# Performance work log

Hardware: AMD Instinct MI355X
Metric: run time of the kernel (lower is better)

The kernel has to match this reference:

```python
import jax, jax.numpy as jnp
import numpy as np
from jax import lax

# shifts generated by _generate_shifts(kernel_size=3): (s1, s2) pairs with
# (s1, s2) >= (0, 0) lexicographically, excluding (0, 0)
SHIFTS = [(0, 1), (1, -1), (1, 0), (1, 1)]


def conv2d_same(x, w, b):
    # x: (B, C_in, H, W), w: (C_out, C_in, kH, kW), b: (C_out,)
    y = lax.conv_general_dilated(
        x, w, window_strides=(1, 1), padding='SAME',
        dimension_numbers=('NCHW', 'OIHW', 'NCHW'))
    return y + b[None, :, None, None]


def setup_inputs() -> dict:
    key = jax.random.key(0)
    k1, k2, k3, k4, k5 = jax.random.split(key, 5)
    B, C_in, C_out, H, W, K = 8, 64, 64, 256, 256, 3
    fan = C_in * K * K
    return {
        'x': jax.random.normal(k1, (B, C_in, H, W), dtype=jnp.float32),
        'w1': jax.random.normal(k2, (C_out, C_in, K, K), dtype=jnp.float32) / np.sqrt(fan),
        'b1': jax.random.normal(k3, (C_out,), dtype=jnp.float32) * 0.01,
        'w2': jax.random.normal(k4, (C_out, C_in, K, K), dtype=jnp.float32) / np.sqrt(fan),
        'b2': jax.random.normal(k5, (C_out,), dtype=jnp.float32) * 0.01,
    }


def reference(x, w1, b1, w2, b2):
    linear_term = conv2d_same(x, w1, b1)
    # torch.roll(x, shifts=(shift_y, shift_x), dims=(2,3)) with
    # circular_shift(x, s1, s2) -> shift_x=s1, shift_y=s2.
    # conv2 is linear, so sum_i conv2(prod_i) == conv2(sum_i prod_i)
    # with the bias added once per shift.
    quad_in = jnp.zeros_like(x)
    for s1, s2 in SHIFTS:
        x_shifted = jnp.roll(x, shift=(s2, s1), axis=(2, 3))
        quad_in = quad_in + jnp.clip(x * x_shifted, -1.0, 1.0)
    quadratic_term = conv2d_same(quad_in, w2, b2 * float(len(SHIFTS)))
    return linear_term + quadratic_term
```

## Files before the change

kernel.cpp:

```cpp
#include <hip/hip_runtime.h>
#include <stdint.h>


typedef short s16x8 __attribute__((ext_vector_type(8)));
typedef float f32x4 __attribute__((ext_vector_type(4)));

__device__ __forceinline__ float clip1(float v) { return fminf(fmaxf(v, -1.f), 1.f); }

__device__ __forceinline__ unsigned short f2bf(float f) {
    union { float f; unsigned u; } v; v.f = f;
    unsigned u = v.u;
    return (unsigned short)((u + 0x7fffu + ((u >> 16) & 1u)) >> 16);
}

__device__ __forceinline__ float bf2f(unsigned short u) {
    union { unsigned v; float f; } t; t.v = ((unsigned)u) << 16; return t.f;
}

__device__ __forceinline__ void gload16(const void* g, void* l) {
    __builtin_amdgcn_global_load_lds(
        (const __attribute__((address_space(1))) unsigned int*)g,
        (__attribute__((address_space(3))) unsigned int*)l, 16, 0, 0);
}

__global__ void prep_w(const float* __restrict__ w1, const float* __restrict__ w2,
                       unsigned short* __restrict__ Wb) {
    int idx = blockIdx.x * 256 + threadIdx.x;
    int kk = idx % 96;
    int rest = idx / 96;
    int co = rest & 63; rest >>= 6;
    int cc = rest & 3;
    int kh = rest >> 2;
    int kw = kk >> 5;
    int cci = kk & 31;
    int c2 = cc * 32 + cci;
    const float* src = (c2 < 64) ? w1 : w2;
    int ci = c2 & 63;
    Wb[idx] = f2bf(src[((co * 64 + ci) * 3 + kh) * 3 + kw]);
}

__global__ __launch_bounds__(512, 1) void prep_u2(const float* __restrict__ x,
                                                  unsigned short* __restrict__ U) {
    __shared__ unsigned short X[3][64][268];
    int bid = blockIdx.x;
    int bh = ((bid & 7) << 8) + (bid >> 3);
    int b = bh >> 8, h = bh & 255;
    int tid = threadIdx.x;

    for (int it = 0; it < 24; ++it) {
        int idx = tid + (it << 9);
        int w4 = idx & 63;
        int c  = (idx >> 6) & 63;
        int r  = idx >> 12;
        int gr = (h + r + 255) & 255;
        const float4 v = *(const float4*)(x + (((size_t)(b * 64 + c)) << 16)
                                            + (gr << 8) + (w4 << 2));
        ushort4 p;
        p.x = f2bf(v.x); p.y = f2bf(v.y); p.z = f2bf(v.z); p.w = f2bf(v.w);
        *(ushort4*)&X[r][c][w4 << 2] = p;
    }
    __syncthreads();

    int c  = tid & 63;
    int wv = tid >> 6;
    int p0 = wv << 5;
    int pm0 = (p0 + 255) & 255;
    float pxc = bf2f(X[1][c][pm0]);
    float pxu = bf2f(X[0][c][pm0]);
    float pxd = bf2f(X[2][c][pm0]);
    size_t base = ((size_t)bh) << 8;
#pragma unroll 4
    for (int i = 0; i < 32; ++i) {
        int p = p0 + i;
        unsigned short xcb = X[1][c][p];
        float xc = bf2f(xcb);
        float xu = bf2f(X[0][c][p]);
        float xd = bf2f(X[2][c][p]);
        float q = clip1(xc * xu) + clip1(xc * pxd) + clip1(xc * pxc) + clip1(xc * pxu);
        size_t po = (base + p) << 7;
        U[po + c]      = xcb;
        U[po + 64 + c] = f2bf(q);
        pxc = xc; pxu = xu; pxd = xd;
    }
}

__global__ __launch_bounds__(512, 2) void conv6(
        const unsigned short* __restrict__ U,
        const unsigned short* __restrict__ Wb,
        const float* __restrict__ b1, const float* __restrict__ b2,
        float* __restrict__ out) {
    __shared__ unsigned short Alds[3][64][96];
    __shared__ unsigned short Ib[2][6][130][32];

    int bid = blockIdx.x;
    int logical = ((bid & 7) << 7) + (bid >> 3);
    int b = logical >> 7;
    int rem = logical & 127;
    int h0 = (rem >> 1) << 2;
    int whalf = rem & 1;
    int w0 = whalf << 7;
    int tid = threadIdx.x;
    int wid = tid >> 6;
    int ln = tid & 63;
    int lr = ln & 15;
    int lq = ln >> 4;
    int rowsel = wid >> 1;
    int pq = wid & 1;
    int o = h0 + rowsel;

    const size_t ubase = ((size_t)b) << 23;

    f32x4 acc[4][4];
#pragma unroll
    for (int m = 0; m < 4; m++)
#pragma unroll
        for (int n = 0; n < 4; n++) {
            acc[m][n][0] = 0.f; acc[m][n][1] = 0.f; acc[m][n][2] = 0.f; acc[m][n][3] = 0.f;
        }

    auto stage_input = [&](int ccx, int nb) {
        const unsigned short* ub = U + ubase + ccx * 32;
#pragma unroll
        for (int ir = 0; ir < 6; ++ir) {
            int r = h0 - 1 + ir;
            if (r < 0 || r > 255) continue;
            int p = 1 + (tid >> 2), q = tid & 3;
            const unsigned short* g = ub + (((size_t)r) << 15)
                                        + (((size_t)(w0 + p - 1)) << 7) + q * 8;
            unsigned short* l = &Ib[nb][ir][1][0] + (size_t)wid * 512;
            gload16(g, l);
        }
    };
    auto stage_weights = [&](int ccx) {
#pragma unroll
        for (int k = 0; k < 5; ++k) {
            int J = k * 512 + tid;
            if (J < 2304) {
                int kh = J / 768;
                int remw = J - kh * 768;
                const unsigned short* g = Wb + (size_t)(kh * 4 + ccx) * 6144 + remw * 8;
                unsigned short* l = ((unsigned short*)Alds) + (size_t)(k * 512 + wid * 64) * 8;
                gload16(g, l);
            }
        }
    };
    auto fix_edges = [&](int ccx, int nb) {
        if (tid < 48) {
            int ir = tid >> 3, rest = tid & 7;
            int side = rest >> 2, q = rest & 3;
            int p = side ? 129 : 0;
            int gcol = side ? (w0 + 128) : (w0 - 1);
            int r = h0 - 1 + ir;
            uint4 v = make_uint4(0u, 0u, 0u, 0u);
            if (gcol >= 0 && gcol <= 255 && r >= 0 && r <= 255)
                v = *(const uint4*)(U + ubase + (((size_t)r) << 15)
                                    + (((size_t)gcol) << 7) + ccx * 32 + q * 8);
            *(uint4*)&Ib[nb][ir][p][q * 8] = v;
        }
        if (h0 == 0)
            for (int i = tid; i < 520; i += 512)
                *(uint4*)&Ib[nb][0][i >> 2][(i & 3) * 8] = make_uint4(0u, 0u, 0u, 0u);
        if (h0 == 252)
            for (int i = tid; i < 520; i += 512)
                *(uint4*)&Ib[nb][5][i >> 2][(i & 3) * 8] = make_uint4(0u, 0u, 0u, 0u);
    };

    stage_input(0, 0);
    stage_weights(0);
    fix_edges(0, 0);
    __syncthreads();

    int cur = 0;
    for (int cc = 0; cc < 4; ++cc) {
        if (cc < 3) stage_input(cc + 1, cur ^ 1);
        __builtin_amdgcn_s_setprio(1);
#pragma unroll
        for (int kh = 0; kh < 3; ++kh) {
            int ir = rowsel + kh;
#pragma unroll
            for (int kw = 0; kw < 3; ++kw) {
                s16x8 af[4], bfr[4];
#pragma unroll
                for (int m = 0; m < 4; m++)
                    af[m] = *(const s16x8*)&Alds[kh][m * 16 + lr][kw * 32 + lq * 8];
#pragma unroll
                for (int n = 0; n < 4; n++)
                    bfr[n] = *(const s16x8*)&Ib[cur][ir][(pq << 6) + n * 16 + lr + kw][lq * 8];
#pragma unroll
                for (int m = 0; m < 4; m++)
#pragma unroll
                    for (int n = 0; n < 4; n++)
                        acc[m][n] = __builtin_amdgcn_mfma_f32_16x16x32_bf16(af[m], bfr[n], acc[m][n], 0, 0, 0);
            }
        }
        __builtin_amdgcn_s_setprio(0);
        __syncthreads();
        if (cc < 3) {
            stage_weights(cc + 1);
            fix_edges(cc + 1, cur ^ 1);
            __syncthreads();
            cur ^= 1;
        }
    }

#pragma unroll
    for (int m = 0; m < 4; m++) {
#pragma unroll
        for (int jj = 0; jj < 4; jj++) {
            int co = m * 16 + lq * 4 + jj;
            float bias = b1[co] + 4.f * b2[co];
#pragma unroll
            for (int n = 0; n < 4; n++) {
                int wpix = w0 + (pq << 6) + n * 16 + lr;
                out[(((size_t)(b * 64 + co)) << 16) + (o << 8) + wpix] = acc[m][n][jj] + bias;
            }
        }
    }
}

__global__ void fallback_conv(const float* __restrict__ x,
                              const float* __restrict__ w1, const float* __restrict__ b1,
                              const float* __restrict__ w2, const float* __restrict__ b2,
                              float* __restrict__ out) {
    size_t idx = (size_t)blockIdx.x * 256 + threadIdx.x;
    int w = idx & 255;
    int h = (int)(idx >> 8) & 255;
    int co = (int)(idx >> 16) & 63;
    int b = (int)(idx >> 22);
    float acc = b1[co] + 4.f * b2[co];
    const float* xb = x + (((size_t)b * 64) << 16);
    for (int ci = 0; ci < 64; ci++) {
        const float* xp = xb + (((size_t)ci) << 16);
        for (int kh = 0; kh < 3; kh++) {
            int hh = h + kh - 1;
            if (hh < 0 || hh > 255) continue;
            for (int kw = 0; kw < 3; kw++) {
                int ww = w + kw - 1;
                if (ww < 0 || ww > 255) continue;
                float xv = xp[(hh << 8) + ww];
                float g1 = w1[((co * 64 + ci) * 3 + kh) * 3 + kw];
                float g2 = w2[((co * 64 + ci) * 3 + kh) * 3 + kw];
                int hm = (hh + 255) & 255, hp = (hh + 1) & 255, wm = (ww + 255) & 255;
                float q = clip1(xv * xp[(hm << 8) + ww]) + clip1(xv * xp[(hp << 8) + wm])
                        + clip1(xv * xp[(hh << 8) + wm]) + clip1(xv * xp[(hm << 8) + wm]);
                acc = fmaf(g1, xv, acc);
                acc = fmaf(g2, q, acc);
            }
        }
    }
    out[idx] = acc;
}

extern "C" void kernel_launch(void* const* d_in, const int* in_sizes, int n_in,
                              void* d_out, int out_size, void* d_ws, size_t ws_size,
                              hipStream_t stream) {
    const float* x  = (const float*)d_in[0];
    const float* w1 = (const float*)d_in[1];
    const float* b1 = (const float*)d_in[2];
    const float* w2 = (const float*)d_in[3];
    const float* b2 = (const float*)d_in[4];
    float* out = (float*)d_out;

    const size_t WB_BYTES = 262144;
    const size_t U_BYTES  = (size_t)8 * 256 * 256 * 128 * 2;
    if (ws_size >= WB_BYTES + U_BYTES) {
        unsigned short* Wb = (unsigned short*)d_ws;
        unsigned short* U  = (unsigned short*)((char*)d_ws + WB_BYTES);
        prep_w<<<dim3(288), dim3(256), 0, stream>>>(w1, w2, Wb);
        prep_u2<<<dim3(2048), dim3(512), 0, stream>>>(x, U);
        conv6<<<dim3(1024), dim3(512), 0, stream>>>(U, Wb, b1, b2, out);
    } else {
        fallback_conv<<<dim3(131072), dim3(256), 0, stream>>>(x, w1, b1, w2, b2, out);
    }
}
```

Before: 174.3 us.

## XOR-swizzle LDS layouts for weight and input tiles in conv kernel

```diff
diff --git a/kernel.cpp b/kernel.cpp
--- a/kernel.cpp
+++ b/kernel.cpp
@@ -24,19 +24,23 @@
 }
 
 __global__ void prep_w(const float* __restrict__ w1, const float* __restrict__ w2,
-                       unsigned short* __restrict__ Wb) {
+                       unsigned short* __restrict__ Wb2) {
     int idx = blockIdx.x * 256 + threadIdx.x;
-    int kk = idx % 96;
-    int rest = idx / 96;
-    int co = rest & 63; rest >>= 6;
-    int cc = rest & 3;
-    int kh = rest >> 2;
-    int kw = kk >> 5;
-    int cci = kk & 31;
-    int c2 = cc * 32 + cci;
-    const float* src = (c2 < 64) ? w1 : w2;
-    int ci = c2 & 63;
-    Wb[idx] = f2bf(src[((co * 64 + ci) * 3 + kh) * 3 + kw]);
+    int sh   = idx & 7;
+    int beta = (idx >> 3) & 15;
+    int co   = (idx >> 7) & 63;
+    int cc   = (idx >> 13) & 3;
+    int kh   = idx >> 15;
+    int blk  = beta ^ (co & 7);
+    float val = 0.f;
+    if (blk < 12) {
+        int kw = blk >> 2;
+        int lq = blk & 3;
+        int c2 = cc * 32 + lq * 8 + sh;
+        const float* src = (c2 < 64) ? w1 : w2;
+        val = src[((co * 64 + (c2 & 63)) * 3 + kh) * 3 + kw];
+    }
+    Wb2[idx] = f2bf(val);
 }
 
 __global__ __launch_bounds__(512, 1) void prep_u2(const float* __restrict__ x,
@@ -84,13 +88,13 @@
     }
 }
 
-__global__ __launch_bounds__(512, 2) void conv6(
+__global__ __launch_bounds__(512, 2) void conv7(
         const unsigned short* __restrict__ U,
-        const unsigned short* __restrict__ Wb,
+        const unsigned short* __restrict__ Wb2,
         const float* __restrict__ b1, const float* __restrict__ b2,
         float* __restrict__ out) {
-    __shared__ unsigned short Alds[3][64][96];
-    __shared__ unsigned short Ib[2][6][130][32];
+    __shared__ unsigned short Alds[3][64][128];
+    __shared__ unsigned short Ib[2][6][4160];
 
     int bid = blockIdx.x;
     int logical = ((bid & 7) << 7) + (bid >> 3);
@@ -107,8 +111,15 @@
     int rowsel = wid >> 1;
     int pq = wid & 1;
     int o = h0 + rowsel;
-
     const size_t ubase = ((size_t)b) << 23;
+
+    int D   = 64 + wid * 1024 + ln * 16;
+    int su  = D >> 7;
+    int stv = ((D >> 4) & 7) ^ (su & 7);
+    int sp  = 2 * su + (stv >> 2);
+    int slq = stv & 3;
+    int scol = w0 - 1 + sp;
+    const unsigned short* usrc0 = U + ubase + (((size_t)scol) << 7) + slq * 8;
 
     f32x4 acc[4][4];
 #pragma unroll
@@ -119,50 +130,45 @@
         }
 
     auto stage_input = [&](int ccx, int nb) {
-        const unsigned short* ub = U + ubase + ccx * 32;
 #pragma unroll
         for (int ir = 0; ir < 6; ++ir) {
             int r = h0 - 1 + ir;
             if (r < 0 || r > 255) continue;
-            int p = 1 + (tid >> 2), q = tid & 3;
-            const unsigned short* g = ub + (((size_t)r) << 15)
-                                        + (((size_t)(w0 + p - 1)) << 7) + q * 8;
-            unsigned short* l = &Ib[nb][ir][1][0] + (size_t)wid * 512;
+            const unsigned short* g = usrc0 + (((size_t)r) << 15) + ccx * 32;
+            void* l = (char*)&Ib[nb][ir][0] + 64 + wid * 1024;
             gload16(g, l);
         }
     };
     auto stage_weights = [&](int ccx) {
 #pragma unroll
-        for (int k = 0; k < 5; ++k) {
-            int J = k * 512 + tid;
-            if (J < 2304) {
-                int kh = J / 768;
-                int remw = J - kh * 768;
-                const unsigned short* g = Wb + (size_t)(kh * 4 + ccx) * 6144 + remw * 8;
-                unsigned short* l = ((unsigned short*)Alds) + (size_t)(k * 512 + wid * 64) * 8;
-                gload16(g, l);
-            }
+        for (int k = 0; k < 6; ++k) {
+            int j = k * 512 + tid;
+            int kh = j >> 10;
+            int remw = j & 1023;
+            const unsigned short* g = Wb2 + (((size_t)(kh * 4 + ccx)) << 13) + remw * 8;
+            void* l = (char*)Alds + (size_t)(k * 512 + wid * 64) * 16;
+            gload16(g, l);
         }
     };
     auto fix_edges = [&](int ccx, int nb) {
         if (tid < 48) {
-            int ir = tid >> 3, rest = tid & 7;
-            int side = rest >> 2, q = rest & 3;
-            int p = side ? 129 : 0;
+            int ir = tid >> 3, r2 = tid & 7;
+            int side = r2 >> 2, q = r2 & 3;
             int gcol = side ? (w0 + 128) : (w0 - 1);
             int r = h0 - 1 + ir;
             uint4 v = make_uint4(0u, 0u, 0u, 0u);
             if (gcol >= 0 && gcol <= 255 && r >= 0 && r <= 255)
                 v = *(const uint4*)(U + ubase + (((size_t)r) << 15)
                                     + (((size_t)gcol) << 7) + ccx * 32 + q * 8);
-            *(uint4*)&Ib[nb][ir][p][q * 8] = v;
+            int off = side ? (8192 + (4 + q) * 16) : (q * 16);
+            *(uint4*)((char*)&Ib[nb][ir][0] + off) = v;
         }
         if (h0 == 0)
             for (int i = tid; i < 520; i += 512)
-                *(uint4*)&Ib[nb][0][i >> 2][(i & 3) * 8] = make_uint4(0u, 0u, 0u, 0u);
+                *(uint4*)((char*)&Ib[nb][0][0] + i * 16) = make_uint4(0u, 0u, 0u, 0u);
         if (h0 == 252)
             for (int i = tid; i < 520; i += 512)
-                *(uint4*)&Ib[nb][5][i >> 2][(i & 3) * 8] = make_uint4(0u, 0u, 0u, 0u);
+                *(uint4*)((char*)&Ib[nb][5][0] + i * 16) = make_uint4(0u, 0u, 0u, 0u);
     };
 
     stage_input(0, 0);
@@ -172,20 +178,29 @@
 
     int cur = 0;
     for (int cc = 0; cc < 4; ++cc) {
-        if (cc < 3) stage_input(cc + 1, cur ^ 1);
+        if (cc < 3) {
+            stage_input(cc + 1, cur ^ 1);
+            fix_edges(cc + 1, cur ^ 1);
+        }
         __builtin_amdgcn_s_setprio(1);
 #pragma unroll
         for (int kh = 0; kh < 3; ++kh) {
             int ir = rowsel + kh;
+            const char* ibb = (const char*)&Ib[cur][ir][0];
 #pragma unroll
             for (int kw = 0; kw < 3; ++kw) {
                 s16x8 af[4], bfr[4];
+                int slot = ((kw << 2) | lq) ^ (lr & 7);
 #pragma unroll
                 for (int m = 0; m < 4; m++)
-                    af[m] = *(const s16x8*)&Alds[kh][m * 16 + lr][kw * 32 + lq * 8];
-#pragma unroll
-                for (int n = 0; n < 4; n++)
-                    bfr[n] = *(const s16x8*)&Ib[cur][ir][(pq << 6) + n * 16 + lr + kw][lq * 8];
+                    af[m] = *(const s16x8*)&Alds[kh][m * 16 + lr][slot * 8];
+#pragma unroll
+                for (int n = 0; n < 4; n++) {
+                    int p = (pq << 6) + n * 16 + lr + kw;
+                    int u = p >> 1;
+                    int s = (((p & 1) << 2) | lq) ^ (u & 7);
+                    bfr[n] = *(const s16x8*)(ibb + u * 128 + s * 16);
+                }
 #pragma unroll
                 for (int m = 0; m < 4; m++)
 #pragma unroll
@@ -197,7 +212,6 @@
         __syncthreads();
         if (cc < 3) {
             stage_weights(cc + 1);
-            fix_edges(cc + 1, cur ^ 1);
             __syncthreads();
             cur ^= 1;
         }
@@ -264,11 +278,11 @@
     const size_t WB_BYTES = 262144;
     const size_t U_BYTES  = (size_t)8 * 256 * 256 * 128 * 2;
     if (ws_size >= WB_BYTES + U_BYTES) {
-        unsigned short* Wb = (unsigned short*)d_ws;
-        unsigned short* U  = (unsigned short*)((char*)d_ws + WB_BYTES);
-        prep_w<<<dim3(288), dim3(256), 0, stream>>>(w1, w2, Wb);
+        unsigned short* Wb2 = (unsigned short*)d_ws;
+        unsigned short* U   = (unsigned short*)((char*)d_ws + WB_BYTES);
+        prep_w<<<dim3(384), dim3(256), 0, stream>>>(w1, w2, Wb2);
         prep_u2<<<dim3(2048), dim3(512), 0, stream>>>(x, U);
-        conv6<<<dim3(1024), dim3(512), 0, stream>>>(U, Wb, b1, b2, out);
+        conv7<<<dim3(1024), dim3(512), 0, stream>>>(U, Wb2, b1, b2, out);
     } else {
         fallback_conv<<<dim3(131072), dim3(256), 0, stream>>>(x, w1, b1, w2, b2, out);
     }
```

Measured after the change: 172.8 us. No clear change (-0.9%).

## Shrink conv tile, read weights from global, swizzle LDS input layout

Applied to the files above, without the earlier changes.

```diff
diff --git a/kernel.cpp b/kernel.cpp
--- a/kernel.cpp
+++ b/kernel.cpp
@@ -84,31 +84,32 @@
     }
 }
 
-__global__ __launch_bounds__(512, 2) void conv6(
+__global__ __launch_bounds__(256, 3) void conv8(
         const unsigned short* __restrict__ U,
         const unsigned short* __restrict__ Wb,
         const float* __restrict__ b1, const float* __restrict__ b2,
         float* __restrict__ out) {
-    __shared__ unsigned short Alds[3][64][96];
-    __shared__ unsigned short Ib[2][6][130][32];
+    __shared__ unsigned short Ib[6][2112];
 
     int bid = blockIdx.x;
-    int logical = ((bid & 7) << 7) + (bid >> 3);
-    int b = logical >> 7;
-    int rem = logical & 127;
-    int h0 = (rem >> 1) << 2;
-    int whalf = rem & 1;
-    int w0 = whalf << 7;
+    int logical = ((bid & 7) << 8) + (bid >> 3);
+    int b = logical >> 8;
+    int rem = logical & 255;
+    int h0 = (rem >> 2) << 2;
+    int w0 = (rem & 3) << 6;
     int tid = threadIdx.x;
     int wid = tid >> 6;
     int ln = tid & 63;
     int lr = ln & 15;
     int lq = ln >> 4;
-    int rowsel = wid >> 1;
-    int pq = wid & 1;
-    int o = h0 + rowsel;
-
+    int o = h0 + wid;
     const size_t ubase = ((size_t)b) << 23;
+
+    int D16 = 4 + (wid << 6) + ln;
+    int su  = D16 >> 3;
+    int stv = (D16 & 7) ^ (su & 7);
+    int pp  = 2 * su + (stv >> 2);
+    const size_t colbase = (((size_t)(w0 - 1 + pp)) << 7) + (size_t)((stv & 3) * 8);
 
     f32x4 acc[4][4];
 #pragma unroll
@@ -118,88 +119,71 @@
             acc[m][n][0] = 0.f; acc[m][n][1] = 0.f; acc[m][n][2] = 0.f; acc[m][n][3] = 0.f;
         }
 
-    auto stage_input = [&](int ccx, int nb) {
-        const unsigned short* ub = U + ubase + ccx * 32;
+    auto stage = [&](int ccx) {
 #pragma unroll
         for (int ir = 0; ir < 6; ++ir) {
             int r = h0 - 1 + ir;
             if (r < 0 || r > 255) continue;
-            int p = 1 + (tid >> 2), q = tid & 3;
-            const unsigned short* g = ub + (((size_t)r) << 15)
-                                        + (((size_t)(w0 + p - 1)) << 7) + q * 8;
-            unsigned short* l = &Ib[nb][ir][1][0] + (size_t)wid * 512;
-            gload16(g, l);
-        }
-    };
-    auto stage_weights = [&](int ccx) {
-#pragma unroll
-        for (int k = 0; k < 5; ++k) {
-            int J = k * 512 + tid;
-            if (J < 2304) {
-                int kh = J / 768;
-                int remw = J - kh * 768;
-                const unsigned short* g = Wb + (size_t)(kh * 4 + ccx) * 6144 + remw * 8;
-                unsigned short* l = ((unsigned short*)Alds) + (size_t)(k * 512 + wid * 64) * 8;
-                gload16(g, l);
-            }
-        }
-    };
-    auto fix_edges = [&](int ccx, int nb) {
+            const unsigned short* g = U + ubase + (((size_t)r) << 15) + colbase + ccx * 32;
+            gload16(g, (char*)&Ib[ir][0] + 64 + (wid << 10));
+        }
         if (tid < 48) {
-            int ir = tid >> 3, rest = tid & 7;
-            int side = rest >> 2, q = rest & 3;
-            int p = side ? 129 : 0;
-            int gcol = side ? (w0 + 128) : (w0 - 1);
+            int ir = tid >> 3, r2 = tid & 7;
+            int side = r2 >> 2, q = r2 & 3;
+            int gcol = side ? (w0 + 64) : (w0 - 1);
             int r = h0 - 1 + ir;
             uint4 v = make_uint4(0u, 0u, 0u, 0u);
             if (gcol >= 0 && gcol <= 255 && r >= 0 && r <= 255)
                 v = *(const uint4*)(U + ubase + (((size_t)r) << 15)
                                     + (((size_t)gcol) << 7) + ccx * 32 + q * 8);
-            *(uint4*)&Ib[nb][ir][p][q * 8] = v;
+            *(uint4*)((char*)&Ib[ir][0] + (side ? 4160 : 0) + q * 16) = v;
         }
         if (h0 == 0)
-            for (int i = tid; i < 520; i += 512)
-                *(uint4*)&Ib[nb][0][i >> 2][(i & 3) * 8] = make_uint4(0u, 0u, 0u, 0u);
+            for (int i = tid; i < 264; i += 256)
+                *(uint4*)((char*)&Ib[0][0] + i * 16) = make_uint4(0u, 0u, 0u, 0u);
         if (h0 == 252)
-            for (int i = tid; i < 520; i += 512)
-                *(uint4*)&Ib[nb][5][i >> 2][(i & 3) * 8] = make_uint4(0u, 0u, 0u, 0u);
+            for (int i = tid; i < 264; i += 256)
+                *(uint4*)((char*)&Ib[5][0] + i * 16) = make_uint4(0u, 0u, 0u, 0u);
     };
 
-    stage_input(0, 0);
-    stage_weights(0);
-    fix_edges(0, 0);
+    stage(0);
     __syncthreads();
 
-    int cur = 0;
     for (int cc = 0; cc < 4; ++cc) {
-        if (cc < 3) stage_input(cc + 1, cur ^ 1);
-        __builtin_amdgcn_s_setprio(1);
 #pragma unroll
         for (int kh = 0; kh < 3; ++kh) {
-            int ir = rowsel + kh;
+            int ir = wid + kh;
+            const char* ibb = (const char*)&Ib[ir][0];
+            const unsigned short* wp = Wb + (size_t)((kh * 4 + cc) * 64) * 96;
+            s16x8 af[3][4];
+#pragma unroll
+            for (int kw = 0; kw < 3; ++kw)
+#pragma unroll
+                for (int m = 0; m < 4; ++m)
+                    af[kw][m] = *(const s16x8*)&wp[(m * 16 + lr) * 96 + kw * 32 + lq * 8];
+            __builtin_amdgcn_s_setprio(1);
 #pragma unroll
             for (int kw = 0; kw < 3; ++kw) {
-                s16x8 af[4], bfr[4];
-#pragma unroll
-                for (int m = 0; m < 4; m++)
-                    af[m] = *(const s16x8*)&Alds[kh][m * 16 + lr][kw * 32 + lq * 8];
-#pragma unroll
-                for (int n = 0; n < 4; n++)
-                    bfr[n] = *(const s16x8*)&Ib[cur][ir][(pq << 6) + n * 16 + lr + kw][lq * 8];
-#pragma unroll
-                for (int m = 0; m < 4; m++)
-#pragma unroll
-                    for (int n = 0; n < 4; n++)
-                        acc[m][n] = __builtin_amdgcn_mfma_f32_16x16x32_bf16(af[m], bfr[n], acc[m][n], 0, 0, 0);
+                s16x8 bfr[4];
+#pragma unroll
+                for (int n = 0; n < 4; ++n) {
+                    int p = n * 16 + lr + kw;
+                    int u = p >> 1;
+                    int s = (((p & 1) << 2) | lq) ^ (u & 7);
+                    bfr[n] = *(const s16x8*)(ibb + u * 128 + s * 16);
+                }
+#pragma unroll
+                for (int m = 0; m < 4; ++m)
+#pragma unroll
+                    for (int n = 0; n < 4; ++n)
+                        acc[m][n] = __builtin_amdgcn_mfma_f32_16x16x32_bf16(af[kw][m], bfr[n], acc[m][n], 0, 0, 0);
             }
-        }
-        __builtin_amdgcn_s_setprio(0);
+            __builtin_amdgcn_s_setprio(0);
+        }
         __syncthreads();
         if (cc < 3) {
-            stage_weights(cc + 1);
-            fix_edges(cc + 1, cur ^ 1);
+            stage(cc + 1);
             __syncthreads();
-            cur ^= 1;
         }
     }
 
@@ -211,7 +195,7 @@
             float bias = b1[co] + 4.f * b2[co];
 #pragma unroll
             for (int n = 0; n < 4; n++) {
-                int wpix = w0 + (pq << 6) + n * 16 + lr;
+                int wpix = w0 + n * 16 + lr;
                 out[(((size_t)(b * 64 + co)) << 16) + (o << 8) + wpix] = acc[m][n][jj] + bias;
             }
         }
@@ -268,7 +252,7 @@
         unsigned short* U  = (unsigned short*)((char*)d_ws + WB_BYTES);
         prep_w<<<dim3(288), dim3(256), 0, stream>>>(w1, w2, Wb);
         prep_u2<<<dim3(2048), dim3(512), 0, stream>>>(x, U);
-        conv6<<<dim3(1024), dim3(512), 0, stream>>>(U, Wb, b1, b2, out);
+        conv8<<<dim3(2048), dim3(256), 0, stream>>>(U, Wb, b1, b2, out);
     } else {
         fallback_conv<<<dim3(131072), dim3(256), 0, stream>>>(x, w1, b1, w2, b2, out);
     }
```

Measured after the change: 182.2 us. +4.5%, slower.
